# Performance work log

Hardware: AMD Instinct MI355X
Metric: run time of the kernel (lower is better)

The kernel has to match this reference:

```python
import jax, jax.numpy as jnp
import numpy as np

B, T, E, D = 8, 2048, 2048, 256  # batch, seq (== max_seq_len), embed_size, block_size

def setup_inputs() -> dict:
    key = jax.random.key(0)
    kx, kq, kk, kv = jax.random.split(key, 4)
    x = jax.random.normal(kx, (B, T, E), dtype=jnp.float32)
    s = 1.0 / np.sqrt(E)
    Wq = jax.random.normal(kq, (E, D), dtype=jnp.float32) * s
    Wk = jax.random.normal(kk, (E, D), dtype=jnp.float32) * s
    Wv = jax.random.normal(kv, (E, D), dtype=jnp.float32) * s
    return {"x": x, "Wq": Wq, "Wk": Wk, "Wv": Wv}

def reference(x, Wq, Wk, Wv):
    # q,k,v: [B, T, D]
    q = jnp.einsum('bte,ed->btd', x, Wq)
    k = jnp.einsum('bte,ed->btd', x, Wk)
    v = jnp.einsum('bte,ed->btd', x, Wv)
    scores = jnp.einsum('bqd,bkd->bqk', q, k)  # [B, T, T]
    causal = jnp.tril(jnp.ones((T, T), dtype=bool))
    scores = jnp.where(causal, scores, -jnp.inf)
    inv_sqrt_d = 1.0 / np.sqrt(D).astype(np.float32)
    # Original divides by sqrt(D) twice: once before softmax, once inside -> net 1/D scale
    scores = scores * inv_sqrt_d
    attn = jax.nn.softmax(scores * inv_sqrt_d, axis=-1)
    z = jnp.einsum('bqk,bkd->bqd', attn, v)
    return z
```

## Files before the change

kernel.cpp:

```cpp
#include <hip/hip_runtime.h>
#include <hip/hip_bf16.h>

typedef unsigned short u16;
typedef unsigned int u32;
typedef __attribute__((ext_vector_type(8))) __bf16 bf16x8;
typedef __attribute__((ext_vector_type(4))) float f32x4;
typedef __attribute__((ext_vector_type(16))) float f32x16;
typedef __attribute__((ext_vector_type(2))) unsigned u32x2;
typedef __attribute__((ext_vector_type(4))) unsigned short u16x4;

__device__ __forceinline__ u16 f2bf(float f) {
  u32 u = __builtin_bit_cast(u32, f);
  return (u16)((u + 0x7fffu + ((u >> 16) & 1u)) >> 16);
}
__device__ __forceinline__ float bf2f(u16 h) {
  u32 u = ((u32)h) << 16;
  return __builtin_bit_cast(float, u);
}
__device__ __forceinline__ u32 pk2(float lo, float hi) {
  union { __bf16 b[2]; u32 u; } r;
  r.b[0] = (__bf16)lo; r.b[1] = (__bf16)hi;
  return r.u;
}

__device__ __forceinline__ void pl32pair(u32& a, u32& b) {
#if __has_builtin(__builtin_amdgcn_permlane32_swap)
  u32x2 r = __builtin_amdgcn_permlane32_swap(a, b, 0, 0);
  a = r.x; b = r.y;
#else
  int hi = (int)((threadIdx.x & 63) >> 5);
  u32 as = __shfl_xor(a, 32), bs = __shfl_xor(b, 32);
  u32 na = hi ? bs : a;
  u32 nb = hi ? b : as;
  a = na; b = nb;
#endif
}
__device__ __forceinline__ float red_max32(float x) {
  u32 a = __builtin_bit_cast(u32, x), b = __builtin_bit_cast(u32, x);
  pl32pair(a, b);
  return fmaxf(__builtin_bit_cast(float, a), __builtin_bit_cast(float, b));
}
__device__ __forceinline__ float red_sum32(float x) {
  u32 a = __builtin_bit_cast(u32, x), b = __builtin_bit_cast(u32, x);
  pl32pair(a, b);
  return __builtin_bit_cast(float, a) + __builtin_bit_cast(float, b);
}

__global__ __launch_bounds__(256) void cast_x_kernel(const float* __restrict__ x,
                                                     u16* __restrict__ xb) {
  size_t i = ((size_t)blockIdx.x * 256 + threadIdx.x) * 8;
  float4 a = *(const float4*)(x + i);
  float4 b = *(const float4*)(x + i + 4);
  union { u16 h[8]; uint4 v; } o;
  o.h[0] = f2bf(a.x); o.h[1] = f2bf(a.y); o.h[2] = f2bf(a.z); o.h[3] = f2bf(a.w);
  o.h[4] = f2bf(b.x); o.h[5] = f2bf(b.y); o.h[6] = f2bf(b.z); o.h[7] = f2bf(b.w);
  *(uint4*)(xb + i) = o.v;
}

__global__ void cast_w_kernel(const float* __restrict__ Wq, const float* __restrict__ Wk,
                              const float* __restrict__ Wv, u16* __restrict__ wbt) {
  __shared__ float tile[32][33];
  int e0 = blockIdx.x * 32, d0 = blockIdx.y * 32, w = blockIdx.z;
  const float* W = (w == 0) ? Wq : ((w == 1) ? Wk : Wv);
  int x = threadIdx.x, y = threadIdx.y;
#pragma unroll
  for (int j = 0; j < 4; j++)
    tile[y + j * 8][x] = W[(size_t)(e0 + y + j * 8) * 256 + d0 + x];
  __syncthreads();
#pragma unroll
  for (int j = 0; j < 4; j++)
    wbt[(size_t)(w * 256 + d0 + y + j * 8) * 2048 + e0 + x] = f2bf(tile[x][y + j * 8]);
}

__global__ __launch_bounds__(256, 2) void gemm_kernel(const u16* __restrict__ A,
                                                      const u16* __restrict__ Bt,
                                                      u16* __restrict__ qbuf,
                                                      u16* __restrict__ kfrag,
                                                      u16* __restrict__ vfrag) {
  __shared__ __align__(16) u16 As[3][4096];
  __shared__ __align__(16) u16 Bs[3][6144];

  int tid = threadIdx.x;
  int w = tid >> 6, l = tid & 63;
  int lr = l & 15, lg = l >> 4;
  int wm = w >> 1, wn = w & 1;

  int bid = blockIdx.x;
  int xcd = bid & 7;
  int colb = xcd >> 1;
  int rowb = ((xcd & 1) << 6) + (bid >> 3);
  int row0 = rowb * 128, col0 = colb * 192;

  int garow = w * 16 + (l >> 2);
  int scol = ((l & 3) * 8) ^ (((l >> 2) & 3) * 8);
  const u16* ga = A + (size_t)(row0 + garow) * 2048 + scol;
  const u16* gb = Bt + (size_t)(col0 + garow) * 2048 + scol;

  f32x4 acc[4][6];
#pragma unroll
  for (int m = 0; m < 4; m++)
#pragma unroll
    for (int n = 0; n < 6; n++) acc[m][n] = (f32x4){0.f, 0.f, 0.f, 0.f};

  int rcol = (lg * 8) ^ ((lr & 3) * 8);

#define STAGE_A3(ts, bi)                                                               \
  {                                                                                    \
    _Pragma("unroll") for (int c = 0; c < 2; c++)                                      \
        __builtin_amdgcn_global_load_lds(                                              \
            (const __attribute__((address_space(1))) void*)(ga + (size_t)c * 64 * 2048 + (ts) * 32), \
            (__attribute__((address_space(3))) void*)&As[bi][(c * 64 + w * 16) * 32], 16, 0, 0); \
  }
#define STAGE_B3(ts, bi)                                                               \
  {                                                                                    \
    _Pragma("unroll") for (int c = 0; c < 3; c++)                                      \
        __builtin_amdgcn_global_load_lds(                                              \
            (const __attribute__((address_space(1))) void*)(gb + (size_t)c * 64 * 2048 + (ts) * 32), \
            (__attribute__((address_space(3))) void*)&Bs[bi][(c * 64 + w * 16) * 32], 16, 0, 0); \
  }

  STAGE_A3(0, 0); STAGE_B3(0, 0);
  STAGE_A3(1, 1); STAGE_B3(1, 1);
  asm volatile("s_waitcnt vmcnt(5)" ::: "memory");
  __builtin_amdgcn_s_barrier();

  int bi = 0, bp = 2;
  for (int t = 0; t < 64; t++) {
    int ts = (t + 2 <= 63) ? (t + 2) : 63;
    const u16* asb = As[bi];
    const u16* bsb = Bs[bi];

    bf16x8 bfr[6], af0, af1;
#pragma unroll
    for (int n = 0; n < 6; n++)
      bfr[n] = *(const bf16x8*)&bsb[(wn * 96 + n * 16 + lr) * 32 + rcol];
    af0 = *(const bf16x8*)&asb[(wm * 64 + 0 * 16 + lr) * 32 + rcol];
    af1 = *(const bf16x8*)&asb[(wm * 64 + 1 * 16 + lr) * 32 + rcol];
    STAGE_A3(ts, bp);
    __builtin_amdgcn_s_barrier();
    asm volatile("s_waitcnt lgkmcnt(0)" ::: "memory");
    __builtin_amdgcn_sched_barrier(0);
    __builtin_amdgcn_s_setprio(1);
#pragma unroll
    for (int n = 0; n < 6; n++) {
      acc[0][n] = __builtin_amdgcn_mfma_f32_16x16x32_bf16(af0, bfr[n], acc[0][n], 0, 0, 0);
      acc[1][n] = __builtin_amdgcn_mfma_f32_16x16x32_bf16(af1, bfr[n], acc[1][n], 0, 0, 0);
    }
    __builtin_amdgcn_s_setprio(0);
    __builtin_amdgcn_s_barrier();

    bf16x8 af2, af3;
    af2 = *(const bf16x8*)&asb[(wm * 64 + 2 * 16 + lr) * 32 + rcol];
    af3 = *(const bf16x8*)&asb[(wm * 64 + 3 * 16 + lr) * 32 + rcol];
    STAGE_B3(ts, bp);
    __builtin_amdgcn_s_barrier();
    asm volatile("s_waitcnt lgkmcnt(0)" ::: "memory");
    __builtin_amdgcn_sched_barrier(0);
    __builtin_amdgcn_s_setprio(1);
#pragma unroll
    for (int n = 0; n < 6; n++) {
      acc[2][n] = __builtin_amdgcn_mfma_f32_16x16x32_bf16(af2, bfr[n], acc[2][n], 0, 0, 0);
      acc[3][n] = __builtin_amdgcn_mfma_f32_16x16x32_bf16(af3, bfr[n], acc[3][n], 0, 0, 0);
    }
    __builtin_amdgcn_s_setprio(0);
    asm volatile("s_waitcnt vmcnt(5)" ::: "memory");
    __builtin_amdgcn_s_barrier();

    bi = (bi == 2) ? 0 : bi + 1;
    bp = (bp == 2) ? 0 : bp + 1;
  }
#undef STAGE_A3
#undef STAGE_B3

  int crow = row0 + wm * 64;
#pragma unroll
  for (int m = 0; m < 4; m++) {
    int t0 = crow + m * 16 + lg * 4;
    int bb = t0 >> 11, tm0 = t0 & 2047;
#pragma unroll
    for (int n = 0; n < 6; n++) {
      int cb = col0 + wn * 96 + n * 16;
      int c = cb + lr;
      if (cb < 256) {
#pragma unroll
        for (int i = 0; i < 4; i++)
          qbuf[(size_t)(t0 + i) * 256 + c] = f2bf(acc[m][n][i]);
      } else if (cb < 512) {
        int kc = c - 256;
        int kvb = tm0 >> 5;
        int t16 = kc >> 4;
        int lhalf = (kc >> 3) & 1;
        int jj = kc & 7;
        size_t base = ((size_t)((bb * 64 + kvb) * 16 + t16) * 64 + lhalf * 32) * 8 + jj;
#pragma unroll
        for (int i = 0; i < 4; i++)
          kfrag[base + (size_t)((tm0 + i) & 31) * 8] = f2bf(acc[m][n][i]);
      } else {
        int vc = c - 512;
        int kvb = tm0 >> 5;
        int ch = (tm0 >> 4) & 1;
        int lhalf = (tm0 >> 3) & 1;
        int jj = tm0 & 7;
        int dblk = vc >> 5;
        int lane = (vc & 31) + lhalf * 32;
        size_t base = ((size_t)(((bb * 64 + kvb) * 2 + ch) * 8 + dblk) * 64 + lane) * 8 + jj;
        u16x4 pk = {f2bf(acc[m][n][0]), f2bf(acc[m][n][1]),
                    f2bf(acc[m][n][2]), f2bf(acc[m][n][3])};
        *(u16x4*)(vfrag + base) = pk;
      }
    }
  }
}

__global__ __launch_bounds__(512, 2) void attn_kernel(const u16* __restrict__ qbuf,
                                                      const u16* __restrict__ kfrag,
                                                      const u16* __restrict__ vfrag,
                                                      float* __restrict__ out) {
  __shared__ __align__(16) u16 qlds[16 * 512];
  __shared__ float facc[32][264];
  __shared__ float sm[4][32];
  __shared__ float sl[4][32];

  int tid = threadIdx.x;
  int w = tid >> 6, l = tid & 63;
  int ql = l & 31, hi = l >> 5;
  int stream = w & 3, dhalf = w >> 2;
  int bid = blockIdx.x;
  int b = bid & 7;
  int p = bid >> 3;

  for (int tile = 0; tile < 2; tile++) {
    int jt = tile ? p : (63 - p);
    int q0 = jt * 32;

    if (tile) __syncthreads();
#pragma unroll
    for (int c = 0; c < 2; c++) {
      int m = c * 512 + tid;
      int t16 = m >> 6, ll = m & 63;
      const u16* src = qbuf + (size_t)(b * 2048 + q0 + (ll & 31)) * 256 + t16 * 16 + (ll >> 5) * 8;
      union { u16 h[8]; bf16x8 v; } in, ov;
      in.v = *(const bf16x8*)src;
#pragma unroll
      for (int j = 0; j < 8; j++) ov.h[j] = f2bf(bf2f(in.h[j]) * (1.0f / 256.0f));
      *(bf16x8*)&qlds[(t16 * 64 + ll) * 8] = ov.v;
    }
    __syncthreads();

    f32x16 o[4];
#pragma unroll
    for (int d = 0; d < 4; d++)
#pragma unroll
      for (int r = 0; r < 16; r++) o[d][r] = 0.f;
    float mreg = -__builtin_inff(), ell = 0.f;

    for (int jb = stream; jb <= jt; jb += 4) {
      const u16* kb = kfrag + ((size_t)(b * 64 + jb) * 16 * 64 + l) * 8;
      const u16* vb = vfrag + ((size_t)(b * 64 + jb) * 16 * 64 + l) * 8;

      f32x16 sA, sB;
#pragma unroll
      for (int r = 0; r < 16; r++) { sA[r] = 0.f; sB[r] = 0.f; }
#pragma unroll
      for (int g = 0; g < 4; g++) {
        bf16x8 k0 = *(const bf16x8*)(kb + (g * 4 + 0) * 512);
        bf16x8 k1 = *(const bf16x8*)(kb + (g * 4 + 1) * 512);
        bf16x8 k2 = *(const bf16x8*)(kb + (g * 4 + 2) * 512);
        bf16x8 k3 = *(const bf16x8*)(kb + (g * 4 + 3) * 512);
        bf16x8 q0f = *(const bf16x8*)&qlds[((g * 4 + 0) * 64 + l) * 8];
        bf16x8 q1f = *(const bf16x8*)&qlds[((g * 4 + 1) * 64 + l) * 8];
        bf16x8 q2f = *(const bf16x8*)&qlds[((g * 4 + 2) * 64 + l) * 8];
        bf16x8 q3f = *(const bf16x8*)&qlds[((g * 4 + 3) * 64 + l) * 8];
        sA = __builtin_amdgcn_mfma_f32_32x32x16_bf16(k0, q0f, sA, 0, 0, 0);
        sB = __builtin_amdgcn_mfma_f32_32x32x16_bf16(k1, q1f, sB, 0, 0, 0);
        sA = __builtin_amdgcn_mfma_f32_32x32x16_bf16(k2, q2f, sA, 0, 0, 0);
        sB = __builtin_amdgcn_mfma_f32_32x32x16_bf16(k3, q3f, sB, 0, 0, 0);
      }

      bf16x8 ve0[4], ve1[4];
#pragma unroll
      for (int dd = 0; dd < 4; dd++) {
        ve0[dd] = *(const bf16x8*)(vb + (dhalf * 4 + dd) * 512);
        ve1[dd] = *(const bf16x8*)(vb + (8 + dhalf * 4 + dd) * 512);
      }

      float s[16];
#pragma unroll
      for (int r = 0; r < 16; r++) s[r] = sA[r] + sB[r];

      if (jb == jt) {
#pragma unroll
        for (int r = 0; r < 16; r++) {
          int kv = (r & 3) + 8 * (r >> 2) + 4 * hi;
          if (kv > ql) s[r] = -__builtin_inff();
        }
      }

      float mx = s[0];
#pragma unroll
      for (int r = 1; r < 16; r++) mx = fmaxf(mx, s[r]);
      mx = red_max32(mx);
      if (__any(mx > mreg + 8.f)) {
        float mnew = fmaxf(mreg, mx);
        float sf = __expf(mreg - mnew);
        mreg = mnew;
        ell *= sf;
#pragma unroll
        for (int d = 0; d < 4; d++)
#pragma unroll
          for (int r = 0; r < 16; r++) o[d][r] *= sf;
      }
      float pr[16], ps = 0.f;
#pragma unroll
      for (int r = 0; r < 16; r++) { pr[r] = __expf(s[r] - mreg); ps += pr[r]; }
      ell += red_sum32(ps);

      u32 wv[8];
#pragma unroll
      for (int i = 0; i < 8; i++) wv[i] = pk2(pr[2 * i], pr[2 * i + 1]);
      pl32pair(wv[0], wv[2]); pl32pair(wv[1], wv[3]);
      pl32pair(wv[4], wv[6]); pl32pair(wv[5], wv[7]);
      union { u32 u[4]; bf16x8 v; } B0, B1;
      B0.u[0] = wv[0]; B0.u[1] = wv[1]; B0.u[2] = wv[2]; B0.u[3] = wv[3];
      B1.u[0] = wv[4]; B1.u[1] = wv[5]; B1.u[2] = wv[6]; B1.u[3] = wv[7];

#pragma unroll
      for (int dd = 0; dd < 4; dd++) {
        o[dd] = __builtin_amdgcn_mfma_f32_32x32x16_bf16(ve0[dd], B0.v, o[dd], 0, 0, 0);
        o[dd] = __builtin_amdgcn_mfma_f32_32x32x16_bf16(ve1[dd], B1.v, o[dd], 0, 0, 0);
      }
    }

    __syncthreads();
    if (w < 4 && l < 32) { sm[w][l] = mreg; sl[w][l] = ell; }
    __syncthreads();

    float M = fmaxf(fmaxf(sm[0][ql], sm[1][ql]), fmaxf(sm[2][ql], sm[3][ql]));
    float alpha = __expf(mreg - M);

#pragma unroll
    for (int ph = 0; ph < 4; ph++) {
      if (stream == ph) {
#pragma unroll
        for (int dd = 0; dd < 4; dd++)
#pragma unroll
          for (int rq = 0; rq < 4; rq++) {
            int base = (dhalf * 4 + dd) * 32 + 8 * rq + 4 * hi;
            f32x4 v;
#pragma unroll
            for (int i = 0; i < 4; i++) v[i] = alpha * o[dd][rq * 4 + i];
            float* fp = &facc[ql][base];
            if (ph == 0) *(f32x4*)fp = v;
            else {
              f32x4 old = *(const f32x4*)fp;
              *(f32x4*)fp = old + v;
            }
          }
      }
      __syncthreads();
    }

    int r = tid >> 4, lt = tid & 15;
    float Mr = fmaxf(fmaxf(sm[0][r], sm[1][r]), fmaxf(sm[2][r], sm[3][r]));
    float denom = 0.f;
#pragma unroll
    for (int ww = 0; ww < 4; ww++) denom += __expf(sm[ww][r] - Mr) * sl[ww][r];
    float inv = 1.0f / denom;
    float* orow = out + (size_t)(b * 2048 + q0 + r) * 256;
#pragma unroll
    for (int j = 0; j < 4; j++) {
      int c = (lt + j * 16) * 4;
      f32x4 v = *(const f32x4*)&facc[r][c];
      v[0] *= inv; v[1] *= inv; v[2] *= inv; v[3] *= inv;
      *(f32x4*)&orow[c] = v;
    }
  }
}

extern "C" void kernel_launch(void* const* d_in, const int* in_sizes, int n_in,
                              void* d_out, int out_size, void* d_ws, size_t ws_size,
                              hipStream_t stream) {
  (void)in_sizes; (void)n_in; (void)out_size; (void)ws_size;
  const float* x = (const float*)d_in[0];
  const float* Wq = (const float*)d_in[1];
  const float* Wk = (const float*)d_in[2];
  const float* Wv = (const float*)d_in[3];
  float* out = (float*)d_out;

  char* ws = (char*)d_ws;
  u16* xb    = (u16*)(ws);
  u16* wbt   = (u16*)(ws + 67108864);
  u16* qbuf  = (u16*)(ws + 70254592);
  u16* kfrag = (u16*)(ws + 78643200);
  u16* vfrag = (u16*)(ws + 87031808);

  cast_x_kernel<<<16384, 256, 0, stream>>>(x, xb);
  cast_w_kernel<<<dim3(64, 8, 3), dim3(32, 8), 0, stream>>>(Wq, Wk, Wv, wbt);
  gemm_kernel<<<512, 256, 0, stream>>>(xb, wbt, qbuf, kfrag, vfrag);
  attn_kernel<<<256, 512, 0, stream>>>(qbuf, kfrag, vfrag, out);
}
```

Before: 146.0 us.

## Share K tiles across wave halves via LDS and remap GEMM block order

```diff
diff --git a/kernel.cpp b/kernel.cpp
--- a/kernel.cpp
+++ b/kernel.cpp
@@ -87,8 +87,9 @@
 
   int bid = blockIdx.x;
   int xcd = bid & 7;
-  int colb = xcd >> 1;
-  int rowb = ((xcd & 1) << 6) + (bid >> 3);
+  int idx = bid >> 3;
+  int rowb = xcd * 16 + (idx >> 2);
+  int colb = idx & 3;
   int row0 = rowb * 128, col0 = colb * 192;
 
   int garow = w * 16 + (l >> 2);
@@ -217,6 +218,7 @@
                                                       const u16* __restrict__ vfrag,
                                                       float* __restrict__ out) {
   __shared__ __align__(16) u16 qlds[16 * 512];
+  __shared__ __align__(16) u16 klds[4 * 16 * 512];
   __shared__ float facc[32][264];
   __shared__ float sm[4][32];
   __shared__ float sl[4][32];
@@ -254,84 +256,101 @@
       for (int r = 0; r < 16; r++) o[d][r] = 0.f;
     float mreg = -__builtin_inff(), ell = 0.f;
 
-    for (int jb = stream; jb <= jt; jb += 4) {
-      const u16* kb = kfrag + ((size_t)(b * 64 + jb) * 16 * 64 + l) * 8;
-      const u16* vb = vfrag + ((size_t)(b * 64 + jb) * 16 * 64 + l) * 8;
-
-      f32x16 sA, sB;
-#pragma unroll
-      for (int r = 0; r < 16; r++) { sA[r] = 0.f; sB[r] = 0.f; }
-#pragma unroll
-      for (int g = 0; g < 4; g++) {
-        bf16x8 k0 = *(const bf16x8*)(kb + (g * 4 + 0) * 512);
-        bf16x8 k1 = *(const bf16x8*)(kb + (g * 4 + 1) * 512);
-        bf16x8 k2 = *(const bf16x8*)(kb + (g * 4 + 2) * 512);
-        bf16x8 k3 = *(const bf16x8*)(kb + (g * 4 + 3) * 512);
-        bf16x8 q0f = *(const bf16x8*)&qlds[((g * 4 + 0) * 64 + l) * 8];
-        bf16x8 q1f = *(const bf16x8*)&qlds[((g * 4 + 1) * 64 + l) * 8];
-        bf16x8 q2f = *(const bf16x8*)&qlds[((g * 4 + 2) * 64 + l) * 8];
-        bf16x8 q3f = *(const bf16x8*)&qlds[((g * 4 + 3) * 64 + l) * 8];
-        sA = __builtin_amdgcn_mfma_f32_32x32x16_bf16(k0, q0f, sA, 0, 0, 0);
-        sB = __builtin_amdgcn_mfma_f32_32x32x16_bf16(k1, q1f, sB, 0, 0, 0);
-        sA = __builtin_amdgcn_mfma_f32_32x32x16_bf16(k2, q2f, sA, 0, 0, 0);
-        sB = __builtin_amdgcn_mfma_f32_32x32x16_bf16(k3, q3f, sB, 0, 0, 0);
+    int nround = (jt >> 2) + 1;
+    for (int rr = 0; rr < nround; rr++) {
+      int jb = rr * 4 + stream;
+      bool act = (jb <= jt);
+
+      if (w < 4 && act) {
+#pragma unroll
+        for (int t = 0; t < 16; t++)
+          __builtin_amdgcn_global_load_lds(
+              (const __attribute__((address_space(1))) void*)(
+                  kfrag + ((size_t)((b * 64 + jb) * 16 + t) * 64 + l) * 8),
+              (__attribute__((address_space(3))) void*)&klds[(stream * 16 + t) * 512],
+              16, 0, 0);
       }
-
-      bf16x8 ve0[4], ve1[4];
-#pragma unroll
-      for (int dd = 0; dd < 4; dd++) {
-        ve0[dd] = *(const bf16x8*)(vb + (dhalf * 4 + dd) * 512);
-        ve1[dd] = *(const bf16x8*)(vb + (8 + dhalf * 4 + dd) * 512);
-      }
-
-      float s[16];
-#pragma unroll
-      for (int r = 0; r < 16; r++) s[r] = sA[r] + sB[r];
-
-      if (jb == jt) {
-#pragma unroll
-        for (int r = 0; r < 16; r++) {
-          int kv = (r & 3) + 8 * (r >> 2) + 4 * hi;
-          if (kv > ql) s[r] = -__builtin_inff();
+      if (w < 4) asm volatile("s_waitcnt vmcnt(0)" ::: "memory");
+      __syncthreads();
+
+      if (act) {
+        const u16* vb = vfrag + ((size_t)(b * 64 + jb) * 16 * 64 + l) * 8;
+        bf16x8 ve0[4], ve1[4];
+#pragma unroll
+        for (int dd = 0; dd < 4; dd++) {
+          ve0[dd] = *(const bf16x8*)(vb + (dhalf * 4 + dd) * 512);
+          ve1[dd] = *(const bf16x8*)(vb + (8 + dhalf * 4 + dd) * 512);
+        }
+
+        const u16* kl = &klds[(stream * 16 * 64 + l) * 8];
+        f32x16 sA, sB;
+#pragma unroll
+        for (int r = 0; r < 16; r++) { sA[r] = 0.f; sB[r] = 0.f; }
+#pragma unroll
+        for (int g = 0; g < 4; g++) {
+          bf16x8 k0 = *(const bf16x8*)(kl + (g * 4 + 0) * 512);
+          bf16x8 k1 = *(const bf16x8*)(kl + (g * 4 + 1) * 512);
+          bf16x8 k2 = *(const bf16x8*)(kl + (g * 4 + 2) * 512);
+          bf16x8 k3 = *(const bf16x8*)(kl + (g * 4 + 3) * 512);
+          bf16x8 q0f = *(const bf16x8*)&qlds[((g * 4 + 0) * 64 + l) * 8];
+          bf16x8 q1f = *(const bf16x8*)&qlds[((g * 4 + 1) * 64 + l) * 8];
+          bf16x8 q2f = *(const bf16x8*)&qlds[((g * 4 + 2) * 64 + l) * 8];
+          bf16x8 q3f = *(const bf16x8*)&qlds[((g * 4 + 3) * 64 + l) * 8];
+          sA = __builtin_amdgcn_mfma_f32_32x32x16_bf16(k0, q0f, sA, 0, 0, 0);
+          sB = __builtin_amdgcn_mfma_f32_32x32x16_bf16(k1, q1f, sB, 0, 0, 0);
+          sA = __builtin_amdgcn_mfma_f32_32x32x16_bf16(k2, q2f, sA, 0, 0, 0);
+          sB = __builtin_amdgcn_mfma_f32_32x32x16_bf16(k3, q3f, sB, 0, 0, 0);
+        }
+
+        float s[16];
+#pragma unroll
+        for (int r = 0; r < 16; r++) s[r] = sA[r] + sB[r];
+
+        if (jb == jt) {
+#pragma unroll
+          for (int r = 0; r < 16; r++) {
+            int kv = (r & 3) + 8 * (r >> 2) + 4 * hi;
+            if (kv > ql) s[r] = -__builtin_inff();
+          }
+        }
+
+        float mx = s[0];
+#pragma unroll
+        for (int r = 1; r < 16; r++) mx = fmaxf(mx, s[r]);
+        mx = red_max32(mx);
+        if (__any(mx > mreg + 8.f)) {
+          float mnew = fmaxf(mreg, mx);
+          float sf = __expf(mreg - mnew);
+          mreg = mnew;
+          ell *= sf;
+#pragma unroll
+          for (int d = 0; d < 4; d++)
+#pragma unroll
+            for (int r = 0; r < 16; r++) o[d][r] *= sf;
+        }
+        float pr[16], ps = 0.f;
+#pragma unroll
+        for (int r = 0; r < 16; r++) { pr[r] = __expf(s[r] - mreg); ps += pr[r]; }
+        ell += red_sum32(ps);
+
+        u32 wv[8];
+#pragma unroll
+        for (int i = 0; i < 8; i++) wv[i] = pk2(pr[2 * i], pr[2 * i + 1]);
+        pl32pair(wv[0], wv[2]); pl32pair(wv[1], wv[3]);
+        pl32pair(wv[4], wv[6]); pl32pair(wv[5], wv[7]);
+        union { u32 u[4]; bf16x8 v; } B0, B1;
+        B0.u[0] = wv[0]; B0.u[1] = wv[1]; B0.u[2] = wv[2]; B0.u[3] = wv[3];
+        B1.u[0] = wv[4]; B1.u[1] = wv[5]; B1.u[2] = wv[6]; B1.u[3] = wv[7];
+
+#pragma unroll
+        for (int dd = 0; dd < 4; dd++) {
+          o[dd] = __builtin_amdgcn_mfma_f32_32x32x16_bf16(ve0[dd], B0.v, o[dd], 0, 0, 0);
+          o[dd] = __builtin_amdgcn_mfma_f32_32x32x16_bf16(ve1[dd], B1.v, o[dd], 0, 0, 0);
         }
       }
-
-      float mx = s[0];
-#pragma unroll
-      for (int r = 1; r < 16; r++) mx = fmaxf(mx, s[r]);
-      mx = red_max32(mx);
-      if (__any(mx > mreg + 8.f)) {
-        float mnew = fmaxf(mreg, mx);
-        float sf = __expf(mreg - mnew);
-        mreg = mnew;
-        ell *= sf;
-#pragma unroll
-        for (int d = 0; d < 4; d++)
-#pragma unroll
-          for (int r = 0; r < 16; r++) o[d][r] *= sf;
-      }
-      float pr[16], ps = 0.f;
-#pragma unroll
-      for (int r = 0; r < 16; r++) { pr[r] = __expf(s[r] - mreg); ps += pr[r]; }
-      ell += red_sum32(ps);
-
-      u32 wv[8];
-#pragma unroll
-      for (int i = 0; i < 8; i++) wv[i] = pk2(pr[2 * i], pr[2 * i + 1]);
-      pl32pair(wv[0], wv[2]); pl32pair(wv[1], wv[3]);
-      pl32pair(wv[4], wv[6]); pl32pair(wv[5], wv[7]);
-      union { u32 u[4]; bf16x8 v; } B0, B1;
-      B0.u[0] = wv[0]; B0.u[1] = wv[1]; B0.u[2] = wv[2]; B0.u[3] = wv[3];
-      B1.u[0] = wv[4]; B1.u[1] = wv[5]; B1.u[2] = wv[6]; B1.u[3] = wv[7];
-
-#pragma unroll
-      for (int dd = 0; dd < 4; dd++) {
-        o[dd] = __builtin_amdgcn_mfma_f32_32x32x16_bf16(ve0[dd], B0.v, o[dd], 0, 0, 0);
-        o[dd] = __builtin_amdgcn_mfma_f32_32x32x16_bf16(ve1[dd], B1.v, o[dd], 0, 0, 0);
-      }
-    }
-
-    __syncthreads();
+      __syncthreads();
+    }
+
     if (w < 4 && l < 32) { sm[w][l] = mreg; sl[w][l] = ell; }
     __syncthreads();
 
```

New measurement: 140.9 us. 1.04x faster.
